# Kernel optimization log

Measured on AMD Instinct MI355X. Metric: run time of the kernel, lower is better.

## Reference

```python
import jax, jax.numpy as jnp
import numpy as np

DIM = 2048
THRESH = 0.33

def _ternary(w):
    # sign() with dead zone: {-1, 0, +1}; detached from grad (matches torch.no_grad)
    return jax.lax.stop_gradient(jnp.where(jnp.abs(w) < THRESH, 0.0, jnp.sign(w)))

def _bitlinear(x, w, b):
    # F.linear(x, ternary_w, bias): x @ ternary_w.T + b
    return jnp.einsum('bsd,od->bso', x, _ternary(w)) + b

def setup_inputs() -> dict:
    key = jax.random.key(0)
    ks = jax.random.split(key, 6)
    B, S, D = 8, 2048, DIM
    x = jax.random.normal(ks[0], (B, S, D), dtype=jnp.float32)
    h_prev = jax.random.normal(ks[1], (B, S, D), dtype=jnp.float32)
    # BitLinear reset_parameters: uniform(-1, 1); bias zeros
    wf = jax.random.uniform(ks[2], (D, D), minval=-1.0, maxval=1.0, dtype=jnp.float32)
    wc = jax.random.uniform(ks[3], (D, D), minval=-1.0, maxval=1.0, dtype=jnp.float32)
    wg = jax.random.uniform(ks[4], (D, D), minval=-1.0, maxval=1.0, dtype=jnp.float32)
    wo = jax.random.uniform(ks[5], (D, D), minval=-1.0, maxval=1.0, dtype=jnp.float32)
    bf = jnp.zeros((D,), dtype=jnp.float32)
    bc = jnp.zeros((D,), dtype=jnp.float32)
    bg = jnp.zeros((D,), dtype=jnp.float32)
    bo = jnp.zeros((D,), dtype=jnp.float32)
    return {"x": x, "h_prev": h_prev, "wf": wf, "bf": bf, "wc": wc, "bc": bc,
            "wg": wg, "bg": bg, "wo": wo, "bo": bo}

def reference(x, h_prev, wf, bf, wc, bc, wg, bg, wo, bo):
    f = jax.nn.sigmoid(_bitlinear(x, wf, bf))
    c = jax.nn.silu(_bitlinear(x, wc, bc))
    h = f * h_prev + (1.0 - f) * c
    g = jax.nn.sigmoid(_bitlinear(x, wg, bg))
    o = _bitlinear(g * h, wo, bo)
    return (o, h)
```

## Files before the change

kernel.cpp:

```cpp
#include <hip/hip_runtime.h>
#include <hip/hip_bf16.h>
#include <cstdint>

#define DIM   2048
#define MROWS 16384
#define PLANE (MROWS * (size_t)DIM)

typedef __bf16 bf16x8 __attribute__((ext_vector_type(8)));
typedef float  f32x4  __attribute__((ext_vector_type(4)));
typedef unsigned short u16;
typedef unsigned int   u32;

#define BARRIER() asm volatile("s_barrier" ::: "memory")
#define WAITVM(N) asm volatile("s_waitcnt vmcnt(" #N ")" ::: "memory")


__device__ __forceinline__ u16 ternary_bits(float w) {
    u32 u = __float_as_uint(w);
    u16 s = (u16)((u >> 16) & 0x8000u);
    return (__builtin_fabsf(w) < 0.33f) ? (u16)0 : (u16)(0x3F80u | s);
}

__device__ __forceinline__ u16 f2bf_rne(float f) {
    u32 u = __float_as_uint(f);
    u32 r = (u + 0x7FFFu + ((u >> 16) & 1u)) >> 16;
    return (u16)r;
}

__device__ __forceinline__ float bf2f(u16 v) {
    u32 u = ((u32)v) << 16;
    return __uint_as_float(u);
}

__device__ __forceinline__ void gload16(const void* g, void* l) {
    __builtin_amdgcn_global_load_lds(
        (const __attribute__((address_space(1))) void*)g,
        (__attribute__((address_space(3))) void*)l,
        16, 0, 0);
}


__global__ void prep_weights(const float* __restrict__ wf, const float* __restrict__ wc,
                             const float* __restrict__ wg, const float* __restrict__ wo,
                             u16* __restrict__ out) {
    const float* srcs[4] = {wf, wc, wg, wo};
    const float* src = srcs[blockIdx.y];
    u16* dst = out + (size_t)blockIdx.y * (DIM * DIM);
    int e = (blockIdx.x * 256 + threadIdx.x) * 8;
    float4 v0 = *(const float4*)(src + e);
    float4 v1 = *(const float4*)(src + e + 4);
    ushort4 o0, o1;
    o0.x = ternary_bits(v0.x); o0.y = ternary_bits(v0.y);
    o0.z = ternary_bits(v0.z); o0.w = ternary_bits(v0.w);
    o1.x = ternary_bits(v1.x); o1.y = ternary_bits(v1.y);
    o1.z = ternary_bits(v1.z); o1.w = ternary_bits(v1.w);
    *(ushort4*)(dst + e)     = o0;
    *(ushort4*)(dst + e + 4) = o1;
}

__global__ void cast_x(const float* __restrict__ x, u16* __restrict__ xb) {
    size_t e = ((size_t)blockIdx.x * 256 + threadIdx.x) * 8;
    float4 v0 = *(const float4*)(x + e);
    float4 v1 = *(const float4*)(x + e + 4);
    ushort4 o0, o1;
    o0.x = f2bf_rne(v0.x); o0.y = f2bf_rne(v0.y);
    o0.z = f2bf_rne(v0.z); o0.w = f2bf_rne(v0.w);
    o1.x = f2bf_rne(v1.x); o1.y = f2bf_rne(v1.y);
    o1.z = f2bf_rne(v1.z); o1.w = f2bf_rne(v1.w);
    *(ushort4*)(xb + e)     = o0;
    *(ushort4*)(xb + e + 4) = o1;
}


template<bool PRE>
__global__ __launch_bounds__(512) void gemm8p(
    const u16* __restrict__ Amat,
    const u16* __restrict__ Wmat,
    u16* __restrict__ pf, u16* __restrict__ pc, u16* __restrict__ pg,
    const float* __restrict__ bias, float* __restrict__ oout)
{
    __shared__ __align__(16) u16 lds[65536];

    const int tid  = threadIdx.x;
    const int lane = tid & 63;
    const int wave = tid >> 6;
    const int wm   = wave >> 2;
    const int wn   = wave & 3;

    const int xcd   = blockIdx.x & 7;
    const int inner = blockIdx.x >> 3;
    int mtile, ntile;
    if (PRE) { ntile = xcd * 3 + inner % 3; mtile = inner / 3; }
    else     { ntile = xcd;                 mtile = inner;     }
    const int brow = mtile * 256;
    const int bcol = ntile * 256;

    const int gc4  = (tid & 3) ^ ((tid >> 3) & 3);
    const int fr   = lane & 15;
    const int hi   = lane >> 4;
    const int csw  = (hi ^ ((fr >> 1) & 3)) * 8;

    f32x4 acc[8][4] = {};

    const u16* aSrc = Amat + (size_t)(brow + (tid >> 2)) * DIM;
    const u16* bSrc = Wmat + (size_t)(bcol + (tid >> 2)) * DIM;

    auto stA = [&](int b, int h, int t) {
        const int k0 = t * 64 + h * 32;
        u16* dst = &lds[b * 32768 + h * 16384 + tid * 8];
        gload16(aSrc + k0 + gc4 * 8, dst);
        gload16(aSrc + (size_t)128 * DIM + k0 + gc4 * 8, dst + 4096);
    };
    auto stB = [&](int b, int h, int t) {
        const int k0 = t * 64 + h * 32;
        u16* dst = &lds[b * 32768 + h * 16384 + 8192 + tid * 8];
        gload16(bSrc + k0 + gc4 * 8, dst);
        gload16(bSrc + (size_t)128 * DIM + k0 + gc4 * 8, dst + 4096);
    };

    auto rdA = [&](int b, int h, bf16x8 (&a)[8]) {
        const u16* p = &lds[b * 32768 + h * 16384];
        #pragma unroll
        for (int mi = 0; mi < 8; ++mi)
            a[mi] = *(const bf16x8*)(p + (wm * 128 + mi * 16 + fr) * 32 + csw);
    };
    auto rdB = [&](int b, int h, int nh, bf16x8 (&bb)[2]) {
        const u16* p = &lds[b * 32768 + h * 16384 + 8192];
        #pragma unroll
        for (int j = 0; j < 2; ++j)
            bb[j] = *(const bf16x8*)(p + (wn * 64 + (nh * 2 + j) * 16 + fr) * 32 + csw);
    };
    auto mf = [&](bf16x8 (&a)[8], bf16x8 (&bb)[2], int nh) {
        __builtin_amdgcn_s_setprio(1);
        #pragma unroll
        for (int j = 0; j < 2; ++j)
            #pragma unroll
            for (int mi = 0; mi < 8; ++mi)
                acc[mi][nh * 2 + j] =
                    __builtin_amdgcn_mfma_f32_16x16x32_bf16(a[mi], bb[j], acc[mi][nh * 2 + j], 0, 0, 0);
        __builtin_amdgcn_s_setprio(0);
    };

    bf16x8 a[8], bb[2];

    stA(0, 0, 0); stB(0, 0, 0);
    stA(0, 1, 0); stB(0, 1, 0);
    stA(1, 0, 1); stB(1, 0, 1);
    WAITVM(8);
    BARRIER();

    #pragma unroll 1
    for (int t = 0; t < 30; ++t) {
        const int b = t & 1, bn = b ^ 1;
        rdA(b, 0, a); rdB(b, 0, 0, bb);
        stA(bn, 1, t + 1);
        BARRIER();
        mf(a, bb, 0);
        BARRIER();
        rdB(b, 0, 1, bb);
        stB(bn, 1, t + 1);
        WAITVM(8);
        BARRIER();
        mf(a, bb, 1);
        BARRIER();
        rdA(b, 1, a); rdB(b, 1, 0, bb);
        stA(b, 0, t + 2);
        BARRIER();
        mf(a, bb, 0);
        BARRIER();
        rdB(b, 1, 1, bb);
        stB(b, 0, t + 2);
        WAITVM(8);
        BARRIER();
        mf(a, bb, 1);
        BARRIER();
    }
    {
        rdA(0, 0, a); rdB(0, 0, 0, bb);
        stA(1, 1, 31);
        BARRIER(); mf(a, bb, 0); BARRIER();
        rdB(0, 0, 1, bb);
        stB(1, 1, 31);
        WAITVM(8);
        BARRIER(); mf(a, bb, 1); BARRIER();
        rdA(0, 1, a); rdB(0, 1, 0, bb);
        BARRIER(); mf(a, bb, 0); BARRIER();
        rdB(0, 1, 1, bb);
        WAITVM(4);
        BARRIER(); mf(a, bb, 1); BARRIER();
    }
    {
        rdA(1, 0, a); rdB(1, 0, 0, bb);
        BARRIER(); mf(a, bb, 0); BARRIER();
        rdB(1, 0, 1, bb);
        WAITVM(0);
        BARRIER(); mf(a, bb, 1); BARRIER();
        rdA(1, 1, a); rdB(1, 1, 0, bb);
        BARRIER(); mf(a, bb, 0); BARRIER();
        rdB(1, 1, 1, bb);
        mf(a, bb, 1);
    }

    if (PRE) {
        BARRIER();
        #pragma unroll
        for (int mi = 0; mi < 8; ++mi)
            #pragma unroll
            for (int ni = 0; ni < 4; ++ni)
                #pragma unroll
                for (int j = 0; j < 4; ++j)
                    lds[(wm * 128 + mi * 16 + hi * 4 + j) * 256 + wn * 64 + ni * 16 + fr] =
                        f2bf_rne(acc[mi][ni][j]);
        BARRIER();
        const int gate = bcol >> 11;
        const int colb = bcol & 2047;
        u16* outp = (gate == 0) ? pf : (gate == 1) ? pc : pg;
        const int rr = tid >> 5;
        const int cc = (tid & 31) * 8;
        #pragma unroll
        for (int rg = 0; rg < 16; ++rg) {
            const int row = rg * 16 + rr;
            bf16x8 v = *(const bf16x8*)(&lds[row * 256 + cc]);
            *(bf16x8*)(outp + (size_t)(brow + row) * DIM + colb + cc) = v;
        }
    } else {
        #pragma unroll
        for (int ni = 0; ni < 4; ++ni) {
            const int col = bcol + wn * 64 + ni * 16 + fr;
            const float bv = bias[col];
            #pragma unroll
            for (int mi = 0; mi < 8; ++mi)
                #pragma unroll
                for (int j = 0; j < 4; ++j)
                    oout[(size_t)(brow + wm * 128 + mi * 16 + hi * 4 + j) * DIM + col] =
                        acc[mi][ni][j] + bv;
        }
    }
}


__global__ __launch_bounds__(256) void fuse_gates(
    const u16* __restrict__ pf, const u16* __restrict__ pc, const u16* __restrict__ pg,
    const float* __restrict__ bfv_, const float* __restrict__ bcv_, const float* __restrict__ bgv_,
    const float* __restrict__ hprev,
    float* __restrict__ hout,
    u16* __restrict__ gh)
{
    #pragma unroll 1
    for (int it = 0; it < 4; ++it) {
        const size_t u = (size_t)blockIdx.x * 256 + threadIdx.x + (size_t)it * 1048576;
        const size_t e = u * 8;
        const int col = (int)(e & 2047);

        ushort4 f0 = *(const ushort4*)(pf + e), f1 = *(const ushort4*)(pf + e + 4);
        ushort4 c0 = *(const ushort4*)(pc + e), c1 = *(const ushort4*)(pc + e + 4);
        ushort4 g0 = *(const ushort4*)(pg + e), g1 = *(const ushort4*)(pg + e + 4);
        float4 hp0 = *(const float4*)(hprev + e), hp1 = *(const float4*)(hprev + e + 4);
        float4 bf0 = *(const float4*)(bfv_ + col), bf1 = *(const float4*)(bfv_ + col + 4);
        float4 bc0 = *(const float4*)(bcv_ + col), bc1 = *(const float4*)(bcv_ + col + 4);
        float4 bg0 = *(const float4*)(bgv_ + col), bg1 = *(const float4*)(bgv_ + col + 4);

        float4 h0, h1;
        ushort4 o0, o1;

        #define DO_ELEM(V, HP, PF, PC, PG, BF, BC, BG, OUT)                   \
        {                                                                      \
            float pfv = bf2f(PF) + (BF);                                       \
            float pcv = bf2f(PC) + (BC);                                       \
            float pgv = bf2f(PG) + (BG);                                       \
            float f  = 1.f / (1.f + __expf(-pfv));                             \
            float cc = pcv / (1.f + __expf(-pcv));                             \
            float g  = 1.f / (1.f + __expf(-pgv));                             \
            float hh = f * (HP) + (1.f - f) * cc;                              \
            V = hh;                                                            \
            OUT = f2bf_rne(g * hh);                                            \
        }
        DO_ELEM(h0.x, hp0.x, f0.x, c0.x, g0.x, bf0.x, bc0.x, bg0.x, o0.x);
        DO_ELEM(h0.y, hp0.y, f0.y, c0.y, g0.y, bf0.y, bc0.y, bg0.y, o0.y);
        DO_ELEM(h0.z, hp0.z, f0.z, c0.z, g0.z, bf0.z, bc0.z, bg0.z, o0.z);
        DO_ELEM(h0.w, hp0.w, f0.w, c0.w, g0.w, bf0.w, bc0.w, bg0.w, o0.w);
        DO_ELEM(h1.x, hp1.x, f1.x, c1.x, g1.x, bf1.x, bc1.x, bg1.x, o1.x);
        DO_ELEM(h1.y, hp1.y, f1.y, c1.y, g1.y, bf1.y, bc1.y, bg1.y, o1.y);
        DO_ELEM(h1.z, hp1.z, f1.z, c1.z, g1.z, bf1.z, bc1.z, bg1.z, o1.z);
        DO_ELEM(h1.w, hp1.w, f1.w, c1.w, g1.w, bf1.w, bc1.w, bg1.w, o1.w);
        #undef DO_ELEM

        *(float4*)(hout + e)     = h0;
        *(float4*)(hout + e + 4) = h1;
        *(ushort4*)(gh + e)      = o0;
        *(ushort4*)(gh + e + 4)  = o1;
    }
}

extern "C" void kernel_launch(void* const* d_in, const int* in_sizes, int n_in,
                              void* d_out, int out_size, void* d_ws, size_t ws_size,
                              hipStream_t stream) {
    const float* x  = (const float*)d_in[0];
    const float* hp = (const float*)d_in[1];
    const float* wf = (const float*)d_in[2];
    const float* bf = (const float*)d_in[3];
    const float* wc = (const float*)d_in[4];
    const float* bc = (const float*)d_in[5];
    const float* wg = (const float*)d_in[6];
    const float* bg = (const float*)d_in[7];
    const float* wo = (const float*)d_in[8];
    const float* bo = (const float*)d_in[9];

    float* o_out = (float*)d_out;
    float* h_out = o_out + PLANE;

    u16* w_t  = (u16*)d_ws;
    u16* x_bf = (u16*)((char*)d_ws + 33554432);
    u16* gh   = (u16*)((char*)d_ws + 100663296);

    u16* p_f = (u16*)o_out;
    u16* p_c = p_f + PLANE;

    prep_weights<<<dim3(2048, 4), 256, 0, stream>>>(wf, wc, wg, wo, w_t);
    cast_x<<<dim3(16384), 256, 0, stream>>>(x, x_bf);
    gemm8p<true><<<dim3(1536), 512, 0, stream>>>(x_bf, w_t, p_f, p_c, gh, nullptr, nullptr);
    fuse_gates<<<dim3(4096), 256, 0, stream>>>(p_f, p_c, gh, bf, bc, bg, hp, h_out, gh);
    gemm8p<false><<<dim3(512), 512, 0, stream>>>(gh, w_t + 3 * (size_t)DIM * DIM,
                                                 nullptr, nullptr, nullptr, bo, o_out);
}
```

Baseline: 694.3 us.

## Fuse gate activations into first GEMM computing all three gates per tile

Replaces the wide 3-gate GEMM plus separate elementwise kernel with one GEMM that computes forget, candidate and gate projections for the same output tile using a shared A tile and a triple-buffered K pipeline, then applies sigmoid/silu, the h update and g*h in the epilogue. This removes writing and re-reading the bf16 preactivation planes and one kernel launch. In exchange it holds three accumulator sets (higher register pressure) and uses scattered per-element epilogue loads and stores of hprev, hout and gh.

```diff
diff --git a/kernel.cpp b/kernel.cpp
--- a/kernel.cpp
+++ b/kernel.cpp
@@ -25,11 +25,6 @@
     u32 u = __float_as_uint(f);
     u32 r = (u + 0x7FFFu + ((u >> 16) & 1u)) >> 16;
     return (u16)r;
-}
-
-__device__ __forceinline__ float bf2f(u16 v) {
-    u32 u = ((u32)v) << 16;
-    return __uint_as_float(u);
 }
 
 __device__ __forceinline__ void gload16(const void* g, void* l) {
@@ -72,14 +67,15 @@
 }
 
 
-template<bool PRE>
-__global__ __launch_bounds__(512) void gemm8p(
-    const u16* __restrict__ Amat,
-    const u16* __restrict__ Wmat,
-    u16* __restrict__ pf, u16* __restrict__ pc, u16* __restrict__ pg,
-    const float* __restrict__ bias, float* __restrict__ oout)
+__global__ __launch_bounds__(512) void gemm1f(
+    const u16* __restrict__ xb,
+    const u16* __restrict__ wt,
+    const float* __restrict__ bfv_, const float* __restrict__ bcv_, const float* __restrict__ bgv_,
+    const float* __restrict__ hprev,
+    float* __restrict__ hout,
+    u16* __restrict__ gh)
 {
-    __shared__ __align__(16) u16 lds[65536];
+    __shared__ __align__(16) u16 lds[61440];
 
     const int tid  = threadIdx.x;
     const int lane = tid & 63;
@@ -89,11 +85,135 @@
 
     const int xcd   = blockIdx.x & 7;
     const int inner = blockIdx.x >> 3;
-    int mtile, ntile;
-    if (PRE) { ntile = xcd * 3 + inner % 3; mtile = inner / 3; }
-    else     { ntile = xcd;                 mtile = inner;     }
-    const int brow = mtile * 256;
-    const int bcol = ntile * 256;
+    const int ntile = xcd * 2 + (inner & 1);
+    const int mtile = inner >> 1;
+    const int brow  = mtile * 256;
+    const int bcol  = ntile * 128;
+
+    const int gc4  = (tid & 3) ^ ((tid >> 3) & 3);
+    const int fr   = lane & 15;
+    const int hi   = lane >> 4;
+    const int csw  = (hi ^ ((fr >> 1) & 3)) * 8;
+
+    f32x4 acc[3][8][2] = {};
+
+    auto stA = [&](int so, int h, int call) {
+        const int row = call * 128 + (tid >> 2);
+        gload16(xb + (size_t)(brow + row) * DIM + h * 32 + gc4 * 8,
+                (u16*)&lds[so + call * 4096 + tid * 8]);
+    };
+    auto stB = [&](int so, int h, int g) {
+        const int row = tid >> 2;
+        gload16(wt + (size_t)(g * 2048 + bcol + row) * DIM + h * 32 + gc4 * 8,
+                (u16*)&lds[so + 8192 + g * 4096 + tid * 8]);
+    };
+
+    auto rdA = [&](int so, bf16x8 (&a)[8]) {
+        #pragma unroll
+        for (int mi = 0; mi < 8; ++mi)
+            a[mi] = *(const bf16x8*)(&lds[so + (wm * 128 + mi * 16 + fr) * 32 + csw]);
+    };
+    auto rdB = [&](int so, int g, bf16x8 (&bb)[2]) {
+        #pragma unroll
+        for (int ni = 0; ni < 2; ++ni)
+            bb[ni] = *(const bf16x8*)(&lds[so + 8192 + g * 4096 + (wn * 32 + ni * 16 + fr) * 32 + csw]);
+    };
+
+    bf16x8 a[8], bb[2];
+
+#define MFG(G)                                                                 \
+    __builtin_amdgcn_s_setprio(1);                                             \
+    _Pragma("unroll")                                                          \
+    for (int ni = 0; ni < 2; ++ni)                                             \
+        _Pragma("unroll")                                                      \
+        for (int mi = 0; mi < 8; ++mi)                                         \
+            acc[G][mi][ni] = __builtin_amdgcn_mfma_f32_16x16x32_bf16(          \
+                a[mi], bb[ni], acc[G][mi][ni], 0, 0, 0);                       \
+    __builtin_amdgcn_s_setprio(0);
+
+    int s0 = 0, s1 = 20480, s2 = 40960;
+
+    stA(s0, 0, 0); stA(s0, 0, 1); stB(s0, 0, 0); stB(s0, 0, 1); stB(s0, 0, 2);
+    stA(s1, 1, 0); stA(s1, 1, 1); stB(s1, 1, 0); stB(s1, 1, 1); stB(s1, 1, 2);
+    WAITVM(5);
+    BARRIER();
+
+    #pragma unroll 1
+    for (int h = 0; h < 62; ++h) {
+        rdA(s0, a); rdB(s0, 0, bb);
+        stA(s2, h + 2, 0); stA(s2, h + 2, 1);
+        BARRIER(); MFG(0); BARRIER();
+        rdB(s0, 1, bb);
+        stB(s2, h + 2, 0); stB(s2, h + 2, 1);
+        BARRIER(); MFG(1); BARRIER();
+        rdB(s0, 2, bb);
+        stB(s2, h + 2, 2);
+        WAITVM(5);
+        BARRIER(); MFG(2); BARRIER();
+        int t = s0; s0 = s1; s1 = s2; s2 = t;
+    }
+    {
+        rdA(s0, a); rdB(s0, 0, bb);
+        BARRIER(); MFG(0); BARRIER();
+        rdB(s0, 1, bb);
+        BARRIER(); MFG(1); BARRIER();
+        rdB(s0, 2, bb);
+        WAITVM(0);
+        BARRIER(); MFG(2); BARRIER();
+        int t = s0; s0 = s1; s1 = s2; s2 = t;
+    }
+    {
+        rdA(s0, a); rdB(s0, 0, bb);
+        MFG(0);
+        rdB(s0, 1, bb);
+        MFG(1);
+        rdB(s0, 2, bb);
+        MFG(2);
+    }
+#undef MFG
+
+    #pragma unroll
+    for (int ni = 0; ni < 2; ++ni) {
+        const int col = bcol + wn * 32 + ni * 16 + fr;
+        const float bfv = bfv_[col], bcv = bcv_[col], bgv = bgv_[col];
+        #pragma unroll
+        for (int mi = 0; mi < 8; ++mi) {
+            #pragma unroll
+            for (int j = 0; j < 4; ++j) {
+                const int row = brow + wm * 128 + mi * 16 + hi * 4 + j;
+                const size_t idx = (size_t)row * DIM + col;
+                float pf = acc[0][mi][ni][j] + bfv;
+                float pc = acc[1][mi][ni][j] + bcv;
+                float pg = acc[2][mi][ni][j] + bgv;
+                float f  = 1.f / (1.f + __expf(-pf));
+                float cc = pc / (1.f + __expf(-pc));
+                float g  = 1.f / (1.f + __expf(-pg));
+                float hh = f * hprev[idx] + (1.f - f) * cc;
+                hout[idx] = hh;
+                gh[idx] = f2bf_rne(g * hh);
+            }
+        }
+    }
+}
+
+
+__global__ __launch_bounds__(512) void gemm2o(
+    const u16* __restrict__ Amat,
+    const u16* __restrict__ Wmat,
+    const float* __restrict__ bias, float* __restrict__ oout)
+{
+    __shared__ __align__(16) u16 lds[65536];
+
+    const int tid  = threadIdx.x;
+    const int lane = tid & 63;
+    const int wave = tid >> 6;
+    const int wm   = wave >> 2;
+    const int wn   = wave & 3;
+
+    const int xcd   = blockIdx.x & 7;
+    const int inner = blockIdx.x >> 3;
+    const int brow  = inner * 256;
+    const int bcol  = xcd * 256;
 
     const int gc4  = (tid & 3) ^ ((tid >> 3) & 3);
     const int fr   = lane & 15;
@@ -154,26 +274,18 @@
         const int b = t & 1, bn = b ^ 1;
         rdA(b, 0, a); rdB(b, 0, 0, bb);
         stA(bn, 1, t + 1);
-        BARRIER();
-        mf(a, bb, 0);
-        BARRIER();
+        BARRIER(); mf(a, bb, 0); BARRIER();
         rdB(b, 0, 1, bb);
         stB(bn, 1, t + 1);
         WAITVM(8);
-        BARRIER();
-        mf(a, bb, 1);
-        BARRIER();
+        BARRIER(); mf(a, bb, 1); BARRIER();
         rdA(b, 1, a); rdB(b, 1, 0, bb);
         stA(b, 0, t + 2);
-        BARRIER();
-        mf(a, bb, 0);
-        BARRIER();
+        BARRIER(); mf(a, bb, 0); BARRIER();
         rdB(b, 1, 1, bb);
         stB(b, 0, t + 2);
         WAITVM(8);
-        BARRIER();
-        mf(a, bb, 1);
-        BARRIER();
+        BARRIER(); mf(a, bb, 1); BARRIER();
     }
     {
         rdA(0, 0, a); rdB(0, 0, 0, bb);
@@ -201,94 +313,16 @@
         mf(a, bb, 1);
     }
 
-    if (PRE) {
-        BARRIER();
+    #pragma unroll
+    for (int ni = 0; ni < 4; ++ni) {
+        const int col = bcol + wn * 64 + ni * 16 + fr;
+        const float bv = bias[col];
         #pragma unroll
         for (int mi = 0; mi < 8; ++mi)
             #pragma unroll
-            for (int ni = 0; ni < 4; ++ni)
-                #pragma unroll
-                for (int j = 0; j < 4; ++j)
-                    lds[(wm * 128 + mi * 16 + hi * 4 + j) * 256 + wn * 64 + ni * 16 + fr] =
-                        f2bf_rne(acc[mi][ni][j]);
-        BARRIER();
-        const int gate = bcol >> 11;
-        const int colb = bcol & 2047;
-        u16* outp = (gate == 0) ? pf : (gate == 1) ? pc : pg;
-        const int rr = tid >> 5;
-        const int cc = (tid & 31) * 8;
-        #pragma unroll
-        for (int rg = 0; rg < 16; ++rg) {
-            const int row = rg * 16 + rr;
-            bf16x8 v = *(const bf16x8*)(&lds[row * 256 + cc]);
-            *(bf16x8*)(outp + (size_t)(brow + row) * DIM + colb + cc) = v;
-        }
-    } else {
-        #pragma unroll
-        for (int ni = 0; ni < 4; ++ni) {
-            const int col = bcol + wn * 64 + ni * 16 + fr;
-            const float bv = bias[col];
-            #pragma unroll
-            for (int mi = 0; mi < 8; ++mi)
-                #pragma unroll
-                for (int j = 0; j < 4; ++j)
-                    oout[(size_t)(brow + wm * 128 + mi * 16 + hi * 4 + j) * DIM + col] =
-                        acc[mi][ni][j] + bv;
-        }
-    }
-}
-
-
-__global__ __launch_bounds__(256) void fuse_gates(
-    const u16* __restrict__ pf, const u16* __restrict__ pc, const u16* __restrict__ pg,
-    const float* __restrict__ bfv_, const float* __restrict__ bcv_, const float* __restrict__ bgv_,
-    const float* __restrict__ hprev,
-    float* __restrict__ hout,
-    u16* __restrict__ gh)
-{
-    #pragma unroll 1
-    for (int it = 0; it < 4; ++it) {
-        const size_t u = (size_t)blockIdx.x * 256 + threadIdx.x + (size_t)it * 1048576;
-        const size_t e = u * 8;
-        const int col = (int)(e & 2047);
-
-        ushort4 f0 = *(const ushort4*)(pf + e), f1 = *(const ushort4*)(pf + e + 4);
-        ushort4 c0 = *(const ushort4*)(pc + e), c1 = *(const ushort4*)(pc + e + 4);
-        ushort4 g0 = *(const ushort4*)(pg + e), g1 = *(const ushort4*)(pg + e + 4);
-        float4 hp0 = *(const float4*)(hprev + e), hp1 = *(const float4*)(hprev + e + 4);
-        float4 bf0 = *(const float4*)(bfv_ + col), bf1 = *(const float4*)(bfv_ + col + 4);
-        float4 bc0 = *(const float4*)(bcv_ + col), bc1 = *(const float4*)(bcv_ + col + 4);
-        float4 bg0 = *(const float4*)(bgv_ + col), bg1 = *(const float4*)(bgv_ + col + 4);
-
-        float4 h0, h1;
-        ushort4 o0, o1;
-
-        #define DO_ELEM(V, HP, PF, PC, PG, BF, BC, BG, OUT)                   \
-        {                                                                      \
-            float pfv = bf2f(PF) + (BF);                                       \
-            float pcv = bf2f(PC) + (BC);                                       \
-            float pgv = bf2f(PG) + (BG);                                       \
-            float f  = 1.f / (1.f + __expf(-pfv));                             \
-            float cc = pcv / (1.f + __expf(-pcv));                             \
-            float g  = 1.f / (1.f + __expf(-pgv));                             \
-            float hh = f * (HP) + (1.f - f) * cc;                              \
-            V = hh;                                                            \
-            OUT = f2bf_rne(g * hh);                                            \
-        }
-        DO_ELEM(h0.x, hp0.x, f0.x, c0.x, g0.x, bf0.x, bc0.x, bg0.x, o0.x);
-        DO_ELEM(h0.y, hp0.y, f0.y, c0.y, g0.y, bf0.y, bc0.y, bg0.y, o0.y);
-        DO_ELEM(h0.z, hp0.z, f0.z, c0.z, g0.z, bf0.z, bc0.z, bg0.z, o0.z);
-        DO_ELEM(h0.w, hp0.w, f0.w, c0.w, g0.w, bf0.w, bc0.w, bg0.w, o0.w);
-        DO_ELEM(h1.x, hp1.x, f1.x, c1.x, g1.x, bf1.x, bc1.x, bg1.x, o1.x);
-        DO_ELEM(h1.y, hp1.y, f1.y, c1.y, g1.y, bf1.y, bc1.y, bg1.y, o1.y);
-        DO_ELEM(h1.z, hp1.z, f1.z, c1.z, g1.z, bf1.z, bc1.z, bg1.z, o1.z);
-        DO_ELEM(h1.w, hp1.w, f1.w, c1.w, g1.w, bf1.w, bc1.w, bg1.w, o1.w);
-        #undef DO_ELEM
-
-        *(float4*)(hout + e)     = h0;
-        *(float4*)(hout + e + 4) = h1;
-        *(ushort4*)(gh + e)      = o0;
-        *(ushort4*)(gh + e + 4)  = o1;
+            for (int j = 0; j < 4; ++j)
+                oout[(size_t)(brow + wm * 128 + mi * 16 + hi * 4 + j) * DIM + col] =
+                    acc[mi][ni][j] + bv;
     }
 }
 
@@ -313,13 +347,8 @@
     u16* x_bf = (u16*)((char*)d_ws + 33554432);
     u16* gh   = (u16*)((char*)d_ws + 100663296);
 
-    u16* p_f = (u16*)o_out;
-    u16* p_c = p_f + PLANE;
-
     prep_weights<<<dim3(2048, 4), 256, 0, stream>>>(wf, wc, wg, wo, w_t);
     cast_x<<<dim3(16384), 256, 0, stream>>>(x, x_bf);
-    gemm8p<true><<<dim3(1536), 512, 0, stream>>>(x_bf, w_t, p_f, p_c, gh, nullptr, nullptr);
-    fuse_gates<<<dim3(4096), 256, 0, stream>>>(p_f, p_c, gh, bf, bc, bg, hp, h_out, gh);
-    gemm8p<false><<<dim3(512), 512, 0, stream>>>(gh, w_t + 3 * (size_t)DIM * DIM,
-                                                 nullptr, nullptr, nullptr, bo, o_out);
-}
+    gemm1f<<<dim3(1024), 512, 0, stream>>>(x_bf, w_t, bf, bc, bg, hp, h_out, gh);
+    gemm2o<<<dim3(512), 512, 0, stream>>>(gh, w_t + 3 * (size_t)DIM * DIM, bo, o_out);
+}
```

Result: slower. 738.9 us (+6.4%).
